# Optimization experiments

Hardware: AMD Instinct MI355X
Metric: run time of the kernel (lower is better)

Reference implementation:

```python
import jax, jax.numpy as jnp
import numpy as np
from jax import lax

V, H, M, OD, NL, S, B, KS = 32000, 1024, 16, 16, 4, 512, 16, 3
N = H // M          # 64
DN = OD * N         # 1024 (layernorm dim)
EPS = 1e-5


def _layernorm(x, g, b):
    mu = jnp.mean(x, axis=-1, keepdims=True)
    var = jnp.var(x, axis=-1, keepdims=True)
    return (x - mu) * lax.rsqrt(var + EPS) * g + b


def _conv(x, w, b):
    y = lax.conv_general_dilated(x, w, (1, 1), 'SAME',
                                 dimension_numbers=('NCHW', 'OIHW', 'NCHW'))
    return y + b[None, :, None, None]


def setup_inputs() -> dict:
    key = jax.random.key(0)
    ks = jax.random.split(key, 16)
    inp = {
        'x': jax.random.randint(ks[0], (B, S), 0, V),
        'emb_table': jax.random.normal(ks[1], (V, H), jnp.float32) * 0.02,
        'ln0_g': jnp.ones((H,), jnp.float32),
        'ln0_b': jnp.zeros((H,), jnp.float32),
        'qw': jax.random.normal(ks[2], (NL, OD, M, KS, KS), jnp.float32) * 0.05,
        'qb': jnp.zeros((NL, OD), jnp.float32),
        'kw': jax.random.normal(ks[3], (NL, OD, M, KS, KS), jnp.float32) * 0.05,
        'kb': jnp.zeros((NL, OD), jnp.float32),
        'vw': jax.random.normal(ks[4], (NL, OD, M, KS, KS), jnp.float32) * 0.05,
        'vb': jnp.zeros((NL, OD), jnp.float32),
        'lng': jnp.ones((NL, DN), jnp.float32),
        'lnb': jnp.zeros((NL, DN), jnp.float32),
        'cw': jax.random.normal(ks[5], (NL, M, OD, 3, 3), jnp.float32) * 0.05,
        'cb': jnp.zeros((NL, M), jnp.float32),
    }
    return inp


def reference(x, emb_table, ln0_g, ln0_b, qw, qb, kw, kb, vw, vb, lng, lnb, cw, cb):
    gelu = lambda t: jax.nn.gelu(t, approximate=False)  # torch nn.GELU default (erf)
    # embedding with padding_idx=0 (row forced to zero)
    table = emb_table.at[0].set(0.0)
    h = _layernorm(table[x], ln0_g, ln0_b)              # [B,S,H]
    h = h.reshape(B, S, M, N).transpose(0, 2, 1, 3)      # [B,M,S,N]
    outs = ()
    for i in range(NL):
        outs = outs + (h,)
        q = gelu(_conv(h, qw[i], qb[i]))                 # [B,OD,S,N]
        k = gelu(_conv(h, kw[i], kb[i]))
        v = gelu(_conv(h, vw[i], vb[i]))
        q2 = q.transpose(0, 2, 1, 3).reshape(B, S, DN)   # [B,S,OD*N]
        k2 = k.transpose(0, 1, 3, 2).reshape(B, DN, S)   # [B,OD*N,S]
        v2 = v.transpose(0, 2, 1, 3).reshape(B, S, DN)
        score = jax.nn.softmax(jnp.matmul(q2, k2), axis=0)  # softmax over batch (dim=0)
        o = jnp.matmul(score, v2)                        # [B,S,DN]
        o = _layernorm(o, lng[i], lnb[i])
        o = o.reshape(B, S, OD, N).transpose(0, 2, 1, 3)  # [B,OD,S,N]
        h = gelu(_conv(o, cw[i], cb[i])) + h             # residual, [B,M,S,N]
    return (h,) + outs
```

## Files before the change

### kernel.cpp

```cpp
#include <hip/hip_runtime.h>
#include <hip/hip_bf16.h>

typedef unsigned short u16;
typedef unsigned int   u32;
typedef short bf16x8 __attribute__((ext_vector_type(8)));
typedef float f32x4  __attribute__((ext_vector_type(4)));

#define SS 512
#define XSWZ(g) ((((g) & 7) << 6) | ((g) >> 3))

__device__ __forceinline__ float gelu_f(float v){
    float x  = v * 0.70710678118654752f;
    float ax = fabsf(x);
    float t  = __builtin_amdgcn_rcpf(fmaf(0.3275911f, ax, 1.0f));
    float poly = t*(0.254829592f + t*(-0.284496736f + t*(1.421413741f
               + t*(-1.453152027f + t*1.061405429f))));
    float e  = __expf(-x*x);
    float er = copysignf(1.0f - poly*e, x);
    return 0.5f*v*(1.0f + er);
}
__device__ __forceinline__ u16 bf16_rne(float v){
    u32 u = __float_as_uint(v);
    u32 r = u + 0x7FFF + ((u >> 16) & 1);
    return (u16)(r >> 16);
}
#define DYT(t) ((t)>=9 ? 0 : (t)/3)
#define DXT(t) ((t)>=9 ? 0 : (t)%3)

__global__ __launch_bounds__(256) void k_embed_ln(
    const int* __restrict__ x, const float* __restrict__ emb,
    const float* __restrict__ g, const float* __restrict__ bta,
    float* __restrict__ h, u16* __restrict__ hh, u16* __restrict__ hl)
{
    int bs = blockIdx.x;
    int b = bs >> 9, s = bs & 511;
    int t = x[bs];
    int tid = threadIdx.x;
    float v[4];
    #pragma unroll
    for (int j = 0; j < 4; ++j){
        int idx = tid + j*256;
        v[j] = (t == 0) ? 0.0f : emb[(size_t)t*1024 + idx];
    }
    float sum = v[0]+v[1]+v[2]+v[3];
    float sq  = v[0]*v[0]+v[1]*v[1]+v[2]*v[2]+v[3]*v[3];
    __shared__ float red[2][4];
    int lane = tid & 63, wid = tid >> 6;
    #pragma unroll
    for (int off = 32; off; off >>= 1){
        sum += __shfl_down(sum, off, 64);
        sq  += __shfl_down(sq,  off, 64);
    }
    if (lane == 0){ red[0][wid] = sum; red[1][wid] = sq; }
    __syncthreads();
    sum = red[0][0]+red[0][1]+red[0][2]+red[0][3];
    sq  = red[1][0]+red[1][1]+red[1][2]+red[1][3];
    float mean = sum * (1.0f/1024.0f);
    float var  = sq  * (1.0f/1024.0f) - mean*mean;
    float rs = rsqrtf(var + 1e-5f);
    #pragma unroll
    for (int j = 0; j < 4; ++j){
        int idx = tid + j*256;
        float y = (v[j]-mean)*rs*g[idx] + bta[idx];
        int m = idx >> 6, n = idx & 63;
        h[((size_t)(b*16 + m)*SS + s)*64 + n] = y;
        u16 hv = bf16_rne(y);
        u16 lv = bf16_rne(y - __uint_as_float((u32)hv<<16));
        size_t da = ((size_t)b*SS + s)*1024 + n*16 + m;
        hh[da] = hv; hl[da] = lv;
    }
}

__global__ __launch_bounds__(512,1) void k_conv_qkv(
    const u16* __restrict__ inh, const u16* __restrict__ inl,
    const float* __restrict__ qw, const float* __restrict__ qb,
    const float* __restrict__ kw, const float* __restrict__ kb,
    const float* __restrict__ vw, const float* __restrict__ vb,
    u16* __restrict__ qoh, u16* __restrict__ qol,
    u16* __restrict__ koh, u16* __restrict__ kol,
    u16* __restrict__ vT)
{
    int bid = XSWZ(blockIdx.x);
    int b  = bid >> 5;
    int y0 = (bid & 31) * 16;
    int tid = threadIdx.x;
    int w8 = tid >> 6, lane = tid & 63;
    int l15 = lane & 15, l4 = lane >> 4;
    int xt = w8 & 3, yh8 = (w8 >> 2) * 8;

    __shared__ u16 wq_h[2560], wq_l[2560], wk_h[2560], wk_l[2560], wv_h[2560];
    __shared__ u16 shi[18*68*24];
    __shared__ u16 slo[18*68*24];

    for (int idx = tid; idx < 2304; idx += 512){
        int o = idx / 144, rem = idx - o*144;
        int i = rem / 9, tap = rem - i*9;
        int dst = o*160 + tap*16 + i;
        float w0 = qw[idx];
        u16 h0 = bf16_rne(w0);
        wq_h[dst] = h0; wq_l[dst] = bf16_rne(w0 - __uint_as_float((u32)h0<<16));
        float w1 = kw[idx];
        u16 h1 = bf16_rne(w1);
        wk_h[dst] = h1; wk_l[dst] = bf16_rne(w1 - __uint_as_float((u32)h1<<16));
        wv_h[dst] = bf16_rne(vw[idx]);
    }
    if (tid < 256){
        int o = tid >> 4, kk = tid & 15;
        int dst = o*160 + 144 + kk;
        wq_h[dst]=0; wq_l[dst]=0; wk_h[dst]=0; wk_l[dst]=0; wv_h[dst]=0;
    }
    if (tid < 72){
        int y = tid >> 2, rr = tid & 3;
        int tc = (rr >> 1) ? 65 : 0;
        int h8 = (rr & 1) * 8;
        int ad = (y*68 + tc)*24 + h8;
        *(uint4*)&shi[ad] = make_uint4(0,0,0,0);
        *(uint4*)&slo[ad] = make_uint4(0,0,0,0);
    }
    for (int idx = tid; idx < 2304; idx += 512){
        int y = idx >> 7;
        int rem = idx & 127;
        int xx = rem >> 1, h8 = (rem & 1)*8;
        int gy = y0 - 1 + y;
        uint4 vh = make_uint4(0,0,0,0), vl = make_uint4(0,0,0,0);
        if (gy >= 0 && gy < SS){
            size_t ga = ((size_t)b*SS + gy)*1024 + xx*16 + h8;
            vh = *(const uint4*)(inh + ga);
            vl = *(const uint4*)(inl + ga);
        }
        int la = (y*68 + (xx+1))*24 + h8;
        *(uint4*)&shi[la] = vh;
        *(uint4*)&slo[la] = vl;
    }
    __syncthreads();

    bf16x8 aq_h[5], aq_l[5], ak_h[5], ak_l[5], av_h[5];
    #pragma unroll
    for (int p = 0; p < 5; ++p){
        int aad = l15*160 + p*32 + l4*8;
        aq_h[p] = *(const bf16x8*)&wq_h[aad];
        aq_l[p] = *(const bf16x8*)&wq_l[aad];
        ak_h[p] = *(const bf16x8*)&wk_h[aad];
        ak_l[p] = *(const bf16x8*)&wk_l[aad];
        av_h[p] = *(const bf16x8*)&wv_h[aad];
    }

    f32x4 accq[8], acck[8], accv[8];
    #pragma unroll
    for (int i = 0; i < 8; ++i){
        accq[i] = (f32x4){0.f,0.f,0.f,0.f};
        acck[i] = (f32x4){0.f,0.f,0.f,0.f};
        accv[i] = (f32x4){0.f,0.f,0.f,0.f};
    }
    int hsel = l4 >> 1;
    int i0 = (l4 & 1)*8;
    int xo = xt*16 + l15;

    #pragma unroll
    for (int p = 0; p < 5; ++p){
        int dy = hsel ? DYT(2*p+1) : DYT(2*p);
        int dx = hsel ? DXT(2*p+1) : DXT(2*p);
        int badd0 = ((dy + yh8)*68 + xo + dx)*24 + i0;
        #pragma unroll
        for (int yy = 0; yy < 8; ++yy){
            int bad = badd0 + yy*(68*24);
            bf16x8 bh = *(const bf16x8*)&shi[bad];
            bf16x8 bl = *(const bf16x8*)&slo[bad];
            accq[yy] = __builtin_amdgcn_mfma_f32_16x16x32_bf16(aq_h[p], bh, accq[yy],0,0,0);
            accq[yy] = __builtin_amdgcn_mfma_f32_16x16x32_bf16(aq_l[p], bh, accq[yy],0,0,0);
            accq[yy] = __builtin_amdgcn_mfma_f32_16x16x32_bf16(aq_h[p], bl, accq[yy],0,0,0);
            acck[yy] = __builtin_amdgcn_mfma_f32_16x16x32_bf16(ak_h[p], bh, acck[yy],0,0,0);
            acck[yy] = __builtin_amdgcn_mfma_f32_16x16x32_bf16(ak_l[p], bh, acck[yy],0,0,0);
            acck[yy] = __builtin_amdgcn_mfma_f32_16x16x32_bf16(ak_h[p], bl, acck[yy],0,0,0);
            accv[yy] = __builtin_amdgcn_mfma_f32_16x16x32_bf16(av_h[p], bh, accv[yy],0,0,0);
        }
    }

    float qbv[4], kbv[4], vbv[4];
    #pragma unroll
    for (int i = 0; i < 4; ++i){
        qbv[i] = qb[l4*4 + i];
        kbv[i] = kb[l4*4 + i];
        vbv[i] = vb[l4*4 + i];
    }
    union { u16 u[4][8]; uint4 q[4]; } vpk;
    #pragma unroll
    for (int yy = 0; yy < 8; ++yy){
        int y = y0 + yh8 + yy;
        u16 qh4[4], ql4[4], kh4[4], kl4[4];
        #pragma unroll
        for (int i = 0; i < 4; ++i){
            float vq = gelu_f(accq[yy][i] + qbv[i]);
            u16 hv = bf16_rne(vq);
            qh4[i] = hv; ql4[i] = bf16_rne(vq - __uint_as_float((u32)hv<<16));
            float vk = gelu_f(acck[yy][i] + kbv[i]);
            u16 kv = bf16_rne(vk);
            kh4[i] = kv; kl4[i] = bf16_rne(vk - __uint_as_float((u32)kv<<16));
            vpk.u[i][yy] = bf16_rne(gelu_f(accv[yy][i] + vbv[i]));
        }
        size_t oa = ((size_t)b*SS + y)*1024 + xo*16 + l4*4;
        *(uint2*)&qoh[oa] = make_uint2((u32)qh4[0]|((u32)qh4[1]<<16),(u32)qh4[2]|((u32)qh4[3]<<16));
        *(uint2*)&qol[oa] = make_uint2((u32)ql4[0]|((u32)ql4[1]<<16),(u32)ql4[2]|((u32)ql4[3]<<16));
        *(uint2*)&koh[oa] = make_uint2((u32)kh4[0]|((u32)kh4[1]<<16),(u32)kh4[2]|((u32)kh4[3]<<16));
        *(uint2*)&kol[oa] = make_uint2((u32)kl4[0]|((u32)kl4[1]<<16),(u32)kl4[2]|((u32)kl4[3]<<16));
    }
    #pragma unroll
    for (int i = 0; i < 4; ++i)
        *(uint4*)(vT + ((size_t)b*1024 + xo*16 + l4*4 + i)*SS + y0 + yh8) = vpk.q[i];
}

__global__ __launch_bounds__(512,1) void k_conv_ln_res2(
    const float* __restrict__ o_pre, const float* __restrict__ stats,
    const float* __restrict__ g, const float* __restrict__ bta,
    const float* __restrict__ w, const float* __restrict__ bias,
    const float* __restrict__ resid, float* __restrict__ outf,
    u16* __restrict__ outh, u16* __restrict__ outl)
{
    int bid = XSWZ(blockIdx.x);
    int b  = bid >> 5;
    int y0 = (bid & 31) * 16;
    int tid = threadIdx.x;
    int w8 = tid >> 6, lane = tid & 63;
    int l15 = lane & 15, l4 = lane >> 4;
    int xt = w8 & 3, yh8 = (w8 >> 2) * 8;

    __shared__ u16 whi[2560], wlo[2560];
    __shared__ u16 shi[18*68*24], slo[18*68*24];
    __shared__ float grem[1024], brem[1024];
    __shared__ float smu[18], srs[18];

    for (int idx = tid; idx < 2304; idx += 512){
        int o = idx / 144, rem = idx - o*144;
        int i = rem / 9, tap = rem - i*9;
        float wv = w[idx];
        u16 hv = bf16_rne(wv);
        int dst = o*160 + tap*16 + i;
        whi[dst] = hv;
        wlo[dst] = bf16_rne(wv - __uint_as_float((u32)hv<<16));
    }
    if (tid < 256){
        int o = tid >> 4, kk = tid & 15;
        whi[o*160 + 144 + kk] = 0;
        wlo[o*160 + 144 + kk] = 0;
    }
    for (int idx = tid; idx < 1024; idx += 512){
        int od = (idx & 15)*64 + (idx >> 4);
        grem[idx] = g[od];
        brem[idx] = bta[od];
    }
    if (tid < 18){
        int gy = y0 - 1 + tid;
        float mu = 0.f, rs = 0.f;
        if (gy >= 0 && gy < SS){
            float s = stats[2*((size_t)b*SS + gy)];
            float q = stats[2*((size_t)b*SS + gy) + 1];
            mu = s * (1.0f/1024.0f);
            float var = q * (1.0f/1024.0f) - mu*mu;
            rs = rsqrtf(var + 1e-5f);
        }
        smu[tid] = mu; srs[tid] = rs;
    }
    if (tid < 72){
        int y = tid >> 2, rr = tid & 3;
        int tc = (rr >> 1) ? 65 : 0;
        int h8 = (rr & 1) * 8;
        int ad = (y*68 + tc)*24 + h8;
        *(uint4*)&shi[ad] = make_uint4(0,0,0,0);
        *(uint4*)&slo[ad] = make_uint4(0,0,0,0);
    }
    __syncthreads();

    for (int idx = tid; idx < 4608; idx += 512){
        int y = idx >> 8;
        int rem = idx & 255;
        int xx = rem >> 2, cq = (rem & 3)*4;
        int gy = y0 - 1 + y;
        int la = (y*68 + xx + 1)*24 + cq;
        if (gy >= 0 && gy < SS){
            float4 vv = *(const float4*)(o_pre + ((size_t)b*SS + gy)*1024 + xx*16 + cq);
            float mu = smu[y], rs = srs[y];
            int dbase = xx*16 + cq;
            float va[4] = {vv.x, vv.y, vv.z, vv.w};
            u16 hh4[4], ll4[4];
            #pragma unroll
            for (int j = 0; j < 4; ++j){
                float yv = (va[j] - mu)*rs*grem[dbase + j] + brem[dbase + j];
                hh4[j] = bf16_rne(yv);
                ll4[j] = bf16_rne(yv - __uint_as_float((u32)hh4[j]<<16));
            }
            *(uint2*)&shi[la] = make_uint2((u32)hh4[0]|((u32)hh4[1]<<16),(u32)hh4[2]|((u32)hh4[3]<<16));
            *(uint2*)&slo[la] = make_uint2((u32)ll4[0]|((u32)ll4[1]<<16),(u32)ll4[2]|((u32)ll4[3]<<16));
        } else {
            *(uint2*)&shi[la] = make_uint2(0,0);
            *(uint2*)&slo[la] = make_uint2(0,0);
        }
    }
    __syncthreads();

    bf16x8 ah[5], al[5];
    #pragma unroll
    for (int p = 0; p < 5; ++p){
        int aad = l15*160 + p*32 + l4*8;
        ah[p] = *(const bf16x8*)&whi[aad];
        al[p] = *(const bf16x8*)&wlo[aad];
    }

    f32x4 acc[8];
    #pragma unroll
    for (int i = 0; i < 8; ++i) acc[i] = (f32x4){0.f,0.f,0.f,0.f};
    int hsel = l4 >> 1;
    int i0 = (l4 & 1)*8;
    int xo = xt*16 + l15;

    #pragma unroll
    for (int p = 0; p < 5; ++p){
        int dy = hsel ? DYT(2*p+1) : DYT(2*p);
        int dx = hsel ? DXT(2*p+1) : DXT(2*p);
        int badd0 = ((dy + yh8)*68 + xo + dx)*24 + i0;
        #pragma unroll
        for (int yy = 0; yy < 8; ++yy){
            int bad = badd0 + yy*(68*24);
            bf16x8 bh = *(const bf16x8*)&shi[bad];
            bf16x8 bl = *(const bf16x8*)&slo[bad];
            acc[yy] = __builtin_amdgcn_mfma_f32_16x16x32_bf16(ah[p], bh, acc[yy],0,0,0);
            acc[yy] = __builtin_amdgcn_mfma_f32_16x16x32_bf16(al[p], bh, acc[yy],0,0,0);
            acc[yy] = __builtin_amdgcn_mfma_f32_16x16x32_bf16(ah[p], bl, acc[yy],0,0,0);
        }
    }

    float bv[4];
    #pragma unroll
    for (int i = 0; i < 4; ++i) bv[i] = bias[l4*4 + i];
    #pragma unroll
    for (int yy = 0; yy < 8; ++yy){
        int y = y0 + yh8 + yy;
        float r[4];
        #pragma unroll
        for (int i = 0; i < 4; ++i) r[i] = gelu_f(acc[yy][i] + bv[i]);
        #pragma unroll
        for (int i = 0; i < 4; ++i){
            int o = l4*4 + i;
            size_t fa = ((size_t)(b*16 + o)*SS + y)*64 + xo;
            float hv = resid[fa] + r[i];
            outf[fa] = hv;
            r[i] = hv;
        }
        u16 hh_[4], ll_[4];
        #pragma unroll
        for (int i = 0; i < 4; ++i){
            hh_[i] = bf16_rne(r[i]);
            ll_[i] = bf16_rne(r[i] - __uint_as_float((u32)hh_[i]<<16));
        }
        size_t oa = ((size_t)b*SS + y)*1024 + xo*16 + l4*4;
        *(uint2*)&outh[oa] = make_uint2((u32)hh_[0]|((u32)hh_[1]<<16),(u32)hh_[2]|((u32)hh_[3]<<16));
        *(uint2*)&outl[oa] = make_uint2((u32)ll_[0]|((u32)ll_[1]<<16),(u32)ll_[2]|((u32)ll_[3]<<16));
    }
}

__global__ __launch_bounds__(256) void k_qk_mfma(
    const u16* __restrict__ qh, const u16* __restrict__ ql,
    const u16* __restrict__ kh, const u16* __restrict__ kl,
    float* __restrict__ score)
{
    int bid = XSWZ(blockIdx.x);
    int b = bid >> 5;
    int s1_0 = ((bid >> 3) & 3) * 128;
    int s2_0 = (bid & 7) * 64;
    __shared__ u16 Ah[128*64], Al[128*64], Bh[64*64], Bl[64*64];
    int tid = threadIdx.x;
    int w = tid >> 6, lane = tid & 63;
    int l15 = lane & 15, l4 = lane >> 4;
    f32x4 acc[2][4];
    #pragma unroll
    for (int r=0;r<2;++r)
        #pragma unroll
        for(int c=0;c<4;++c) acc[r][c] = (f32x4){0.f,0.f,0.f,0.f};

    for (int oc = 0; oc < 16; ++oc){
        size_t qbase = ((size_t)b*SS + s1_0)*1024 + oc*64;
        size_t kbase = ((size_t)b*SS + s2_0)*1024 + oc*64;
        #pragma unroll
        for (int i = 0; i < 4; ++i){
            int idx = tid + i*256;
            int r = idx >> 3, f = idx & 7;
            int dst = r*64 + ((f ^ (r & 7))*8);
            *(uint4*)&Ah[dst] = *(const uint4*)(qh + qbase + (size_t)r*1024 + f*8);
            *(uint4*)&Al[dst] = *(const uint4*)(ql + qbase + (size_t)r*1024 + f*8);
        }
        #pragma unroll
        for (int i = 0; i < 2; ++i){
            int idx = tid + i*256;
            int r = idx >> 3, f = idx & 7;
            int dst = r*64 + ((f ^ (r & 7))*8);
            *(uint4*)&Bh[dst] = *(const uint4*)(kh + kbase + (size_t)r*1024 + f*8);
            *(uint4*)&Bl[dst] = *(const uint4*)(kl + kbase + (size_t)r*1024 + f*8);
        }
        __syncthreads();
        #pragma unroll
        for (int ks = 0; ks < 2; ++ks){
            bf16x8 a_h[2], a_l[2];
            #pragma unroll
            for (int r=0;r<2;++r){
                int row = w*32 + r*16 + l15;
                int ad = row*64 + (((ks*4 + l4) ^ (row & 7))*8);
                a_h[r] = *(const bf16x8*)&Ah[ad];
                a_l[r] = *(const bf16x8*)&Al[ad];
            }
            #pragma unroll
            for (int c=0;c<4;++c){
                int row = c*16 + l15;
                int bd = row*64 + (((ks*4 + l4) ^ (row & 7))*8);
                bf16x8 b_h = *(const bf16x8*)&Bh[bd];
                bf16x8 b_l = *(const bf16x8*)&Bl[bd];
                #pragma unroll
                for (int r=0;r<2;++r){
                    acc[r][c] = __builtin_amdgcn_mfma_f32_16x16x32_bf16(a_h[r], b_h, acc[r][c],0,0,0);
                    acc[r][c] = __builtin_amdgcn_mfma_f32_16x16x32_bf16(a_l[r], b_h, acc[r][c],0,0,0);
                    acc[r][c] = __builtin_amdgcn_mfma_f32_16x16x32_bf16(a_h[r], b_l, acc[r][c],0,0,0);
                }
            }
        }
        __syncthreads();
    }
    #pragma unroll
    for (int r=0;r<2;++r)
        #pragma unroll
        for (int c=0;c<4;++c)
            #pragma unroll
            for (int i=0;i<4;++i){
                int s1 = s1_0 + w*32 + r*16 + l4*4 + i;
                int s2 = s2_0 + c*16 + l15;
                score[((size_t)b*SS + s1)*SS + s2] = acc[r][c][i];
            }
}

__global__ __launch_bounds__(256) void k_softmax_b(
    const float* __restrict__ score, u16* __restrict__ scb,
    float* __restrict__ stats)
{
    int sid = blockIdx.x*256 + threadIdx.x;
    if (sid < 16384) stats[sid] = 0.0f;
    float vals[16];
    float m = -1e30f;
    #pragma unroll
    for (int b = 0; b < 16; ++b){
        vals[b] = score[(size_t)b*SS*SS + sid];
        m = fmaxf(m, vals[b]);
    }
    float sum = 0.f;
    #pragma unroll
    for (int b = 0; b < 16; ++b){ vals[b] = __expf(vals[b]-m); sum += vals[b]; }
    float inv = 1.0f/sum;
    #pragma unroll
    for (int b = 0; b < 16; ++b) scb[(size_t)b*SS*SS + sid] = bf16_rne(vals[b]*inv);
}

__global__ __launch_bounds__(256) void k_sv_mfma(
    const u16* __restrict__ scb, const u16* __restrict__ vT,
    float* __restrict__ o, float* __restrict__ stats)
{
    int bid = XSWZ(blockIdx.x);
    int b = bid >> 5;
    int s1_0 = ((bid >> 3) & 3) * 128;
    int d0 = (bid & 7) * 128;
    __shared__ u16 As[128*64], Bs[128*64];
    int tid = threadIdx.x;
    int w = tid >> 6, lane = tid & 63;
    int l15 = lane & 15, l4 = lane >> 4;
    f32x4 acc[2][8];
    #pragma unroll
    for (int r=0;r<2;++r)
        #pragma unroll
        for(int c=0;c<8;++c) acc[r][c] = (f32x4){0.f,0.f,0.f,0.f};

    for (int st = 0; st < 8; ++st){
        int s2b = st*64;
        #pragma unroll
        for (int i = 0; i < 4; ++i){
            int idx = tid + i*256;
            int r = idx >> 3, f = idx & 7;
            int dst = r*64 + ((f ^ (r & 7))*8);
            *(uint4*)&As[dst] = *(const uint4*)(scb + ((size_t)b*SS + s1_0 + r)*SS + s2b + f*8);
            *(uint4*)&Bs[dst] = *(const uint4*)(vT + ((size_t)b*1024 + d0 + r)*SS + s2b + f*8);
        }
        __syncthreads();
        #pragma unroll
        for (int ks = 0; ks < 2; ++ks){
            bf16x8 a0[2];
            #pragma unroll
            for (int r=0;r<2;++r){
                int row = w*32 + r*16 + l15;
                a0[r] = *(const bf16x8*)&As[row*64 + (((ks*4 + l4) ^ (row & 7))*8)];
            }
            #pragma unroll
            for (int c=0;c<8;++c){
                int row = c*16 + l15;
                bf16x8 b0 = *(const bf16x8*)&Bs[row*64 + (((ks*4 + l4) ^ (row & 7))*8)];
                #pragma unroll
                for (int r=0;r<2;++r)
                    acc[r][c] = __builtin_amdgcn_mfma_f32_16x16x32_bf16(a0[r], b0, acc[r][c],0,0,0);
            }
        }
        __syncthreads();
    }
    #pragma unroll
    for (int r=0;r<2;++r)
        #pragma unroll
        for (int c=0;c<8;++c)
            #pragma unroll
            for (int i=0;i<4;++i){
                int s1 = s1_0 + w*32 + r*16 + l4*4 + i;
                o[((size_t)b*SS + s1)*1024 + d0 + c*16 + l15] = acc[r][c][i];
            }

    #pragma unroll
    for (int r=0;r<2;++r){
        #pragma unroll
        for (int i=0;i<4;++i){
            float s = 0.f, q = 0.f;
            #pragma unroll
            for (int c=0;c<8;++c){ float v = acc[r][c][i]; s += v; q += v*v; }
            #pragma unroll
            for (int m = 1; m <= 8; m <<= 1){
                s += __shfl_xor(s, m, 64);
                q += __shfl_xor(q, m, 64);
            }
            if (l15 == 0){
                int s1 = s1_0 + w*32 + r*16 + l4*4 + i;
                atomicAdd(&stats[2*((size_t)b*SS + s1)],     s);
                atomicAdd(&stats[2*((size_t)b*SS + s1) + 1], q);
            }
        }
    }
}

extern "C" void kernel_launch(void* const* d_in, const int* in_sizes, int n_in,
                              void* d_out, int out_size, void* d_ws, size_t ws_size,
                              hipStream_t stream)
{
    const int*   x    = (const int*)  d_in[0];
    const float* emb  = (const float*)d_in[1];
    const float* g0   = (const float*)d_in[2];
    const float* b0   = (const float*)d_in[3];
    const float* qw   = (const float*)d_in[4];
    const float* qb   = (const float*)d_in[5];
    const float* kw   = (const float*)d_in[6];
    const float* kb   = (const float*)d_in[7];
    const float* vw   = (const float*)d_in[8];
    const float* vb_  = (const float*)d_in[9];
    const float* lng  = (const float*)d_in[10];
    const float* lnb  = (const float*)d_in[11];
    const float* cw   = (const float*)d_in[12];
    const float* cb   = (const float*)d_in[13];
    float* out = (float*)d_out;

    const size_t TS = (size_t)16*16*512*64;
    u16* wsu = (u16*)d_ws;
    u16* hh = wsu + 0*TS;
    u16* hl = wsu + 1*TS;
    u16* qh = wsu + 2*TS;
    u16* ql = wsu + 3*TS;
    u16* kh = wsu + 4*TS;
    u16* kl = wsu + 5*TS;
    u16* vT = wsu + 6*TS;
    float* sc    = (float*)(wsu + 7*TS);
    u16*   scb   = qh;
    float* o_pre = (float*)(wsu + 4*TS);
    float* stats = (float*)(wsu + 3*TS);

    float* hbuf[5];
    hbuf[0] = out + 1*TS;
    hbuf[1] = out + 2*TS;
    hbuf[2] = out + 3*TS;
    hbuf[3] = out + 4*TS;
    hbuf[4] = out;

    k_embed_ln<<<8192, 256, 0, stream>>>(x, emb, g0, b0, hbuf[0], hh, hl);
    for (int i = 0; i < 4; ++i){
        k_conv_qkv<<<512, 512, 0, stream>>>(
            hh, hl, qw + i*2304, qb + i*16, kw + i*2304, kb + i*16,
            vw + i*2304, vb_ + i*16, qh, ql, kh, kl, vT);
        k_qk_mfma<<<512, 256, 0, stream>>>(qh, ql, kh, kl, sc);
        k_softmax_b<<<1024, 256, 0, stream>>>(sc, scb, stats);
        k_sv_mfma<<<512, 256, 0, stream>>>(scb, vT, o_pre, stats);
        k_conv_ln_res2<<<512, 512, 0, stream>>>(
            o_pre, stats, lng + i*1024, lnb + i*1024, cw + i*2304, cb + i*16,
            hbuf[i], hbuf[i+1], hh, hl);
    }
}
```

Measured before the change: 609.7 us.

## Precompute split-bf16 conv weights once; halve matmul tile height to double grid

Adds a small prep kernel that converts conv weights into hi/lo bf16 in the padded tap layout and permutes the layernorm gamma/beta, once per call for all layers. The two conv kernels then copy these into LDS with vector loads instead of converting per block. The QK and SV matmul kernels now use 64-row tiles instead of 128, launching 1024 blocks instead of 512 to improve occupancy and load balance across CUs, at the cost of reloading the B operand more often. The prep buffer sits at a fixed 160 MB workspace offset, which assumes the workspace is that large.

Result: slower. 671.2 us (+10.1%).

```diff
diff --git a/kernel.cpp b/kernel.cpp
--- a/kernel.cpp
+++ b/kernel.cpp
@@ -7,7 +7,9 @@
 typedef float f32x4  __attribute__((ext_vector_type(4)));
 
 #define SS 512
-#define XSWZ(g) ((((g) & 7) << 6) | ((g) >> 3))
+#define XSWZ(g)     ((((g) & 7) << 6) | ((g) >> 3))
+#define XSWZ1024(g) ((((g) & 7) << 7) | ((g) >> 3))
+#define WPREP_STRIDE 22016
 
 __device__ __forceinline__ float gelu_f(float v){
     float x  = v * 0.70710678118654752f;
@@ -27,6 +29,46 @@
 #define DYT(t) ((t)>=9 ? 0 : (t)/3)
 #define DXT(t) ((t)>=9 ? 0 : (t)%3)
 
+__global__ __launch_bounds__(256) void k_prep(
+    const float* __restrict__ qw, const float* __restrict__ kw,
+    const float* __restrict__ vw, const float* __restrict__ cw,
+    const float* __restrict__ lng, const float* __restrict__ lnb,
+    u16* __restrict__ wprep)
+{
+    int L = blockIdx.x;
+    int tid = threadIdx.x;
+    u16* base = wprep + L*WPREP_STRIDE;
+    const float* src[4] = {qw + L*2304, kw + L*2304, vw + L*2304, cw + L*2304};
+    const int offh[4] = {0, 5120, 10240, 12800};
+    const int offl[4] = {2560, 7680, -1, 15360};
+    for (int idx = tid; idx < 2304; idx += 256){
+        int o = idx / 144, rem = idx - o*144;
+        int i = rem / 9, tap = rem - i*9;
+        int dst = o*160 + tap*16 + i;
+        #pragma unroll
+        for (int a = 0; a < 4; ++a){
+            float wv = src[a][idx];
+            u16 hv = bf16_rne(wv);
+            base[offh[a] + dst] = hv;
+            if (offl[a] >= 0)
+                base[offl[a] + dst] = bf16_rne(wv - __uint_as_float((u32)hv<<16));
+        }
+    }
+    {
+        int o = tid >> 4, kk = tid & 15;
+        int d = o*160 + 144 + kk;
+        base[d]=0; base[2560+d]=0; base[5120+d]=0; base[7680+d]=0;
+        base[10240+d]=0; base[12800+d]=0; base[15360+d]=0;
+    }
+    float* gr = (float*)(base + 17920);
+    float* br = (float*)(base + 19968);
+    for (int idx = tid; idx < 1024; idx += 256){
+        int od = (idx & 15)*64 + (idx >> 4);
+        gr[idx] = lng[L*1024 + od];
+        br[idx] = lnb[L*1024 + od];
+    }
+}
+
 __global__ __launch_bounds__(256) void k_embed_ln(
     const int* __restrict__ x, const float* __restrict__ emb,
     const float* __restrict__ g, const float* __restrict__ bta,
@@ -73,9 +115,9 @@
 
 __global__ __launch_bounds__(512,1) void k_conv_qkv(
     const u16* __restrict__ inh, const u16* __restrict__ inl,
-    const float* __restrict__ qw, const float* __restrict__ qb,
-    const float* __restrict__ kw, const float* __restrict__ kb,
-    const float* __restrict__ vw, const float* __restrict__ vb,
+    const u16* __restrict__ wp,
+    const float* __restrict__ qb, const float* __restrict__ kb,
+    const float* __restrict__ vb,
     u16* __restrict__ qoh, u16* __restrict__ qol,
     u16* __restrict__ koh, u16* __restrict__ kol,
     u16* __restrict__ vT)
@@ -88,26 +130,16 @@
     int l15 = lane & 15, l4 = lane >> 4;
     int xt = w8 & 3, yh8 = (w8 >> 2) * 8;
 
-    __shared__ u16 wq_h[2560], wq_l[2560], wk_h[2560], wk_l[2560], wv_h[2560];
+    __shared__ __align__(16) u16 wq_h[2560], wq_l[2560], wk_h[2560], wk_l[2560], wv_h[2560];
     __shared__ u16 shi[18*68*24];
     __shared__ u16 slo[18*68*24];
 
-    for (int idx = tid; idx < 2304; idx += 512){
-        int o = idx / 144, rem = idx - o*144;
-        int i = rem / 9, tap = rem - i*9;
-        int dst = o*160 + tap*16 + i;
-        float w0 = qw[idx];
-        u16 h0 = bf16_rne(w0);
-        wq_h[dst] = h0; wq_l[dst] = bf16_rne(w0 - __uint_as_float((u32)h0<<16));
-        float w1 = kw[idx];
-        u16 h1 = bf16_rne(w1);
-        wk_h[dst] = h1; wk_l[dst] = bf16_rne(w1 - __uint_as_float((u32)h1<<16));
-        wv_h[dst] = bf16_rne(vw[idx]);
-    }
-    if (tid < 256){
-        int o = tid >> 4, kk = tid & 15;
-        int dst = o*160 + 144 + kk;
-        wq_h[dst]=0; wq_l[dst]=0; wk_h[dst]=0; wk_l[dst]=0; wv_h[dst]=0;
+    if (tid < 320){
+        ((uint4*)wq_h)[tid] = ((const uint4*)(wp        ))[tid];
+        ((uint4*)wq_l)[tid] = ((const uint4*)(wp +  2560))[tid];
+        ((uint4*)wk_h)[tid] = ((const uint4*)(wp +  5120))[tid];
+        ((uint4*)wk_l)[tid] = ((const uint4*)(wp +  7680))[tid];
+        ((uint4*)wv_h)[tid] = ((const uint4*)(wp + 10240))[tid];
     }
     if (tid < 72){
         int y = tid >> 2, rr = tid & 3;
@@ -211,8 +243,7 @@
 
 __global__ __launch_bounds__(512,1) void k_conv_ln_res2(
     const float* __restrict__ o_pre, const float* __restrict__ stats,
-    const float* __restrict__ g, const float* __restrict__ bta,
-    const float* __restrict__ w, const float* __restrict__ bias,
+    const u16* __restrict__ wp, const float* __restrict__ bias,
     const float* __restrict__ resid, float* __restrict__ outf,
     u16* __restrict__ outh, u16* __restrict__ outl)
 {
@@ -224,29 +255,18 @@
     int l15 = lane & 15, l4 = lane >> 4;
     int xt = w8 & 3, yh8 = (w8 >> 2) * 8;
 
-    __shared__ u16 whi[2560], wlo[2560];
+    __shared__ __align__(16) u16 whi[2560], wlo[2560];
     __shared__ u16 shi[18*68*24], slo[18*68*24];
-    __shared__ float grem[1024], brem[1024];
+    __shared__ __align__(16) float grem[1024], brem[1024];
     __shared__ float smu[18], srs[18];
 
-    for (int idx = tid; idx < 2304; idx += 512){
-        int o = idx / 144, rem = idx - o*144;
-        int i = rem / 9, tap = rem - i*9;
-        float wv = w[idx];
-        u16 hv = bf16_rne(wv);
-        int dst = o*160 + tap*16 + i;
-        whi[dst] = hv;
-        wlo[dst] = bf16_rne(wv - __uint_as_float((u32)hv<<16));
+    if (tid < 320){
+        ((uint4*)whi)[tid] = ((const uint4*)(wp + 12800))[tid];
+        ((uint4*)wlo)[tid] = ((const uint4*)(wp + 15360))[tid];
     }
     if (tid < 256){
-        int o = tid >> 4, kk = tid & 15;
-        whi[o*160 + 144 + kk] = 0;
-        wlo[o*160 + 144 + kk] = 0;
-    }
-    for (int idx = tid; idx < 1024; idx += 512){
-        int od = (idx & 15)*64 + (idx >> 4);
-        grem[idx] = g[od];
-        brem[idx] = bta[od];
+        ((float4*)grem)[tid] = ((const float4*)(wp + 17920))[tid];
+        ((float4*)brem)[tid] = ((const float4*)(wp + 19968))[tid];
     }
     if (tid < 18){
         int gy = y0 - 1 + tid;
@@ -260,8 +280,9 @@
         }
         smu[tid] = mu; srs[tid] = rs;
     }
-    if (tid < 72){
-        int y = tid >> 2, rr = tid & 3;
+    if (tid >= 64 && tid < 136){
+        int t2 = tid - 64;
+        int y = t2 >> 2, rr = t2 & 3;
         int tc = (rr >> 1) ? 65 : 0;
         int h8 = (rr & 1) * 8;
         int ad = (y*68 + tc)*24 + h8;
@@ -362,174 +383,150 @@
     const u16* __restrict__ kh, const u16* __restrict__ kl,
     float* __restrict__ score)
 {
-    int bid = XSWZ(blockIdx.x);
-    int b = bid >> 5;
-    int s1_0 = ((bid >> 3) & 3) * 128;
+    int bid = XSWZ1024(blockIdx.x);
+    int b = bid >> 6;
+    int s1_0 = ((bid >> 3) & 7) * 64;
     int s2_0 = (bid & 7) * 64;
-    __shared__ u16 Ah[128*64], Al[128*64], Bh[64*64], Bl[64*64];
+    __shared__ u16 Ah[64*64], Al[64*64], Bh[64*64], Bl[64*64];
     int tid = threadIdx.x;
     int w = tid >> 6, lane = tid & 63;
     int l15 = lane & 15, l4 = lane >> 4;
-    f32x4 acc[2][4];
-    #pragma unroll
-    for (int r=0;r<2;++r)
-        #pragma unroll
-        for(int c=0;c<4;++c) acc[r][c] = (f32x4){0.f,0.f,0.f,0.f};
+    f32x4 acc[4];
+    #pragma unroll
+    for (int c=0;c<4;++c) acc[c] = (f32x4){0.f,0.f,0.f,0.f};
 
     for (int oc = 0; oc < 16; ++oc){
         size_t qbase = ((size_t)b*SS + s1_0)*1024 + oc*64;
         size_t kbase = ((size_t)b*SS + s2_0)*1024 + oc*64;
         #pragma unroll
-        for (int i = 0; i < 4; ++i){
+        for (int i = 0; i < 2; ++i){
             int idx = tid + i*256;
             int r = idx >> 3, f = idx & 7;
             int dst = r*64 + ((f ^ (r & 7))*8);
             *(uint4*)&Ah[dst] = *(const uint4*)(qh + qbase + (size_t)r*1024 + f*8);
             *(uint4*)&Al[dst] = *(const uint4*)(ql + qbase + (size_t)r*1024 + f*8);
-        }
+            *(uint4*)&Bh[dst] = *(const uint4*)(kh + kbase + (size_t)r*1024 + f*8);
+            *(uint4*)&Bl[dst] = *(const uint4*)(kl + kbase + (size_t)r*1024 + f*8);
+        }
+        __syncthreads();
+        #pragma unroll
+        for (int ks = 0; ks < 2; ++ks){
+            int rowa = w*16 + l15;
+            int ad = rowa*64 + (((ks*4 + l4) ^ (rowa & 7))*8);
+            bf16x8 a_h = *(const bf16x8*)&Ah[ad];
+            bf16x8 a_l = *(const bf16x8*)&Al[ad];
+            #pragma unroll
+            for (int c=0;c<4;++c){
+                int rowb = c*16 + l15;
+                int bd = rowb*64 + (((ks*4 + l4) ^ (rowb & 7))*8);
+                bf16x8 b_h = *(const bf16x8*)&Bh[bd];
+                bf16x8 b_l = *(const bf16x8*)&Bl[bd];
+                acc[c] = __builtin_amdgcn_mfma_f32_16x16x32_bf16(a_h, b_h, acc[c],0,0,0);
+                acc[c] = __builtin_amdgcn_mfma_f32_16x16x32_bf16(a_l, b_h, acc[c],0,0,0);
+                acc[c] = __builtin_amdgcn_mfma_f32_16x16x32_bf16(a_h, b_l, acc[c],0,0,0);
+            }
+        }
+        __syncthreads();
+    }
+    #pragma unroll
+    for (int c=0;c<4;++c)
+        #pragma unroll
+        for (int i=0;i<4;++i){
+            int s1 = s1_0 + w*16 + l4*4 + i;
+            int s2 = s2_0 + c*16 + l15;
+            score[((size_t)b*SS + s1)*SS + s2] = acc[c][i];
+        }
+}
+
+__global__ __launch_bounds__(256) void k_softmax_b(
+    const float* __restrict__ score, u16* __restrict__ scb,
+    float* __restrict__ stats)
+{
+    int sid = blockIdx.x*256 + threadIdx.x;
+    if (sid < 16384) stats[sid] = 0.0f;
+    float vals[16];
+    float m = -1e30f;
+    #pragma unroll
+    for (int b = 0; b < 16; ++b){
+        vals[b] = score[(size_t)b*SS*SS + sid];
+        m = fmaxf(m, vals[b]);
+    }
+    float sum = 0.f;
+    #pragma unroll
+    for (int b = 0; b < 16; ++b){ vals[b] = __expf(vals[b]-m); sum += vals[b]; }
+    float inv = 1.0f/sum;
+    #pragma unroll
+    for (int b = 0; b < 16; ++b) scb[(size_t)b*SS*SS + sid] = bf16_rne(vals[b]*inv);
+}
+
+__global__ __launch_bounds__(256) void k_sv_mfma(
+    const u16* __restrict__ scb, const u16* __restrict__ vT,
+    float* __restrict__ o, float* __restrict__ stats)
+{
+    int bid = XSWZ1024(blockIdx.x);
+    int b = bid >> 6;
+    int s1_0 = ((bid >> 3) & 7) * 64;
+    int d0 = (bid & 7) * 128;
+    __shared__ u16 As[64*64], Bs[128*64];
+    int tid = threadIdx.x;
+    int w = tid >> 6, lane = tid & 63;
+    int l15 = lane & 15, l4 = lane >> 4;
+    f32x4 acc[8];
+    #pragma unroll
+    for(int c=0;c<8;++c) acc[c] = (f32x4){0.f,0.f,0.f,0.f};
+
+    for (int st = 0; st < 8; ++st){
+        int s2b = st*64;
         #pragma unroll
         for (int i = 0; i < 2; ++i){
             int idx = tid + i*256;
             int r = idx >> 3, f = idx & 7;
             int dst = r*64 + ((f ^ (r & 7))*8);
-            *(uint4*)&Bh[dst] = *(const uint4*)(kh + kbase + (size_t)r*1024 + f*8);
-            *(uint4*)&Bl[dst] = *(const uint4*)(kl + kbase + (size_t)r*1024 + f*8);
-        }
-        __syncthreads();
-        #pragma unroll
-        for (int ks = 0; ks < 2; ++ks){
-            bf16x8 a_h[2], a_l[2];
-            #pragma unroll
-            for (int r=0;r<2;++r){
-                int row = w*32 + r*16 + l15;
-                int ad = row*64 + (((ks*4 + l4) ^ (row & 7))*8);
-                a_h[r] = *(const bf16x8*)&Ah[ad];
-                a_l[r] = *(const bf16x8*)&Al[ad];
-            }
-            #pragma unroll
-            for (int c=0;c<4;++c){
-                int row = c*16 + l15;
-                int bd = row*64 + (((ks*4 + l4) ^ (row & 7))*8);
-                bf16x8 b_h = *(const bf16x8*)&Bh[bd];
-                bf16x8 b_l = *(const bf16x8*)&Bl[bd];
-                #pragma unroll
-                for (int r=0;r<2;++r){
-                    acc[r][c] = __builtin_amdgcn_mfma_f32_16x16x32_bf16(a_h[r], b_h, acc[r][c],0,0,0);
-                    acc[r][c] = __builtin_amdgcn_mfma_f32_16x16x32_bf16(a_l[r], b_h, acc[r][c],0,0,0);
-                    acc[r][c] = __builtin_amdgcn_mfma_f32_16x16x32_bf16(a_h[r], b_l, acc[r][c],0,0,0);
-                }
-            }
-        }
-        __syncthreads();
-    }
-    #pragma unroll
-    for (int r=0;r<2;++r)
-        #pragma unroll
-        for (int c=0;c<4;++c)
-            #pragma unroll
-            for (int i=0;i<4;++i){
-                int s1 = s1_0 + w*32 + r*16 + l4*4 + i;
-                int s2 = s2_0 + c*16 + l15;
-                score[((size_t)b*SS + s1)*SS + s2] = acc[r][c][i];
-            }
-}
-
-__global__ __launch_bounds__(256) void k_softmax_b(
-    const float* __restrict__ score, u16* __restrict__ scb,
-    float* __restrict__ stats)
-{
-    int sid = blockIdx.x*256 + threadIdx.x;
-    if (sid < 16384) stats[sid] = 0.0f;
-    float vals[16];
-    float m = -1e30f;
-    #pragma unroll
-    for (int b = 0; b < 16; ++b){
-        vals[b] = score[(size_t)b*SS*SS + sid];
-        m = fmaxf(m, vals[b]);
-    }
-    float sum = 0.f;
-    #pragma unroll
-    for (int b = 0; b < 16; ++b){ vals[b] = __expf(vals[b]-m); sum += vals[b]; }
-    float inv = 1.0f/sum;
-    #pragma unroll
-    for (int b = 0; b < 16; ++b) scb[(size_t)b*SS*SS + sid] = bf16_rne(vals[b]*inv);
-}
-
-__global__ __launch_bounds__(256) void k_sv_mfma(
-    const u16* __restrict__ scb, const u16* __restrict__ vT,
-    float* __restrict__ o, float* __restrict__ stats)
-{
-    int bid = XSWZ(blockIdx.x);
-    int b = bid >> 5;
-    int s1_0 = ((bid >> 3) & 3) * 128;
-    int d0 = (bid & 7) * 128;
-    __shared__ u16 As[128*64], Bs[128*64];
-    int tid = threadIdx.x;
-    int w = tid >> 6, lane = tid & 63;
-    int l15 = lane & 15, l4 = lane >> 4;
-    f32x4 acc[2][8];
-    #pragma unroll
-    for (int r=0;r<2;++r)
-        #pragma unroll
-        for(int c=0;c<8;++c) acc[r][c] = (f32x4){0.f,0.f,0.f,0.f};
-
-    for (int st = 0; st < 8; ++st){
-        int s2b = st*64;
+            *(uint4*)&As[dst] = *(const uint4*)(scb + ((size_t)b*SS + s1_0 + r)*SS + s2b + f*8);
+        }
         #pragma unroll
         for (int i = 0; i < 4; ++i){
             int idx = tid + i*256;
             int r = idx >> 3, f = idx & 7;
             int dst = r*64 + ((f ^ (r & 7))*8);
-            *(uint4*)&As[dst] = *(const uint4*)(scb + ((size_t)b*SS + s1_0 + r)*SS + s2b + f*8);
             *(uint4*)&Bs[dst] = *(const uint4*)(vT + ((size_t)b*1024 + d0 + r)*SS + s2b + f*8);
         }
         __syncthreads();
         #pragma unroll
         for (int ks = 0; ks < 2; ++ks){
-            bf16x8 a0[2];
-            #pragma unroll
-            for (int r=0;r<2;++r){
-                int row = w*32 + r*16 + l15;
-                a0[r] = *(const bf16x8*)&As[row*64 + (((ks*4 + l4) ^ (row & 7))*8)];
-            }
+            int rowa = w*16 + l15;
+            bf16x8 a0 = *(const bf16x8*)&As[rowa*64 + (((ks*4 + l4) ^ (rowa & 7))*8)];
             #pragma unroll
             for (int c=0;c<8;++c){
-                int row = c*16 + l15;
-                bf16x8 b0 = *(const bf16x8*)&Bs[row*64 + (((ks*4 + l4) ^ (row & 7))*8)];
-                #pragma unroll
-                for (int r=0;r<2;++r)
-                    acc[r][c] = __builtin_amdgcn_mfma_f32_16x16x32_bf16(a0[r], b0, acc[r][c],0,0,0);
+                int rowb = c*16 + l15;
+                bf16x8 b0 = *(const bf16x8*)&Bs[rowb*64 + (((ks*4 + l4) ^ (rowb & 7))*8)];
+                acc[c] = __builtin_amdgcn_mfma_f32_16x16x32_bf16(a0, b0, acc[c],0,0,0);
             }
         }
         __syncthreads();
     }
     #pragma unroll
-    for (int r=0;r<2;++r)
-        #pragma unroll
-        for (int c=0;c<8;++c)
-            #pragma unroll
-            for (int i=0;i<4;++i){
-                int s1 = s1_0 + w*32 + r*16 + l4*4 + i;
-                o[((size_t)b*SS + s1)*1024 + d0 + c*16 + l15] = acc[r][c][i];
-            }
-
-    #pragma unroll
-    for (int r=0;r<2;++r){
+    for (int c=0;c<8;++c)
         #pragma unroll
         for (int i=0;i<4;++i){
-            float s = 0.f, q = 0.f;
-            #pragma unroll
-            for (int c=0;c<8;++c){ float v = acc[r][c][i]; s += v; q += v*v; }
-            #pragma unroll
-            for (int m = 1; m <= 8; m <<= 1){
-                s += __shfl_xor(s, m, 64);
-                q += __shfl_xor(q, m, 64);
-            }
-            if (l15 == 0){
-                int s1 = s1_0 + w*32 + r*16 + l4*4 + i;
-                atomicAdd(&stats[2*((size_t)b*SS + s1)],     s);
-                atomicAdd(&stats[2*((size_t)b*SS + s1) + 1], q);
-            }
+            int s1 = s1_0 + w*16 + l4*4 + i;
+            o[((size_t)b*SS + s1)*1024 + d0 + c*16 + l15] = acc[c][i];
+        }
+
+    #pragma unroll
+    for (int i=0;i<4;++i){
+        float s = 0.f, q = 0.f;
+        #pragma unroll
+        for (int c=0;c<8;++c){ float v = acc[c][i]; s += v; q += v*v; }
+        #pragma unroll
+        for (int m = 1; m <= 8; m <<= 1){
+            s += __shfl_xor(s, m, 64);
+            q += __shfl_xor(q, m, 64);
+        }
+        if (l15 == 0){
+            int s1 = s1_0 + w*16 + l4*4 + i;
+            atomicAdd(&stats[2*((size_t)b*SS + s1)],     s);
+            atomicAdd(&stats[2*((size_t)b*SS + s1) + 1], q);
         }
     }
 }
@@ -567,6 +564,7 @@
     u16*   scb   = qh;
     float* o_pre = (float*)(wsu + 4*TS);
     float* stats = (float*)(wsu + 3*TS);
+    u16* wprep = (u16*)((char*)d_ws + ((size_t)160 << 20));
 
     float* hbuf[5];
     hbuf[0] = out + 1*TS;
@@ -575,16 +573,16 @@
     hbuf[3] = out + 4*TS;
     hbuf[4] = out;
 
+    k_prep<<<4, 256, 0, stream>>>(qw, kw, vw, cw, lng, lnb, wprep);
     k_embed_ln<<<8192, 256, 0, stream>>>(x, emb, g0, b0, hbuf[0], hh, hl);
     for (int i = 0; i < 4; ++i){
+        const u16* wp = wprep + i*WPREP_STRIDE;
         k_conv_qkv<<<512, 512, 0, stream>>>(
-            hh, hl, qw + i*2304, qb + i*16, kw + i*2304, kb + i*16,
-            vw + i*2304, vb_ + i*16, qh, ql, kh, kl, vT);
-        k_qk_mfma<<<512, 256, 0, stream>>>(qh, ql, kh, kl, sc);
+            hh, hl, wp, qb + i*16, kb + i*16, vb_ + i*16, qh, ql, kh, kl, vT);
+        k_qk_mfma<<<1024, 256, 0, stream>>>(qh, ql, kh, kl, sc);
         k_softmax_b<<<1024, 256, 0, stream>>>(sc, scb, stats);
-        k_sv_mfma<<<512, 256, 0, stream>>>(scb, vT, o_pre, stats);
+        k_sv_mfma<<<1024, 256, 0, stream>>>(scb, vT, o_pre, stats);
         k_conv_ln_res2<<<512, 512, 0, stream>>>(
-            o_pre, stats, lng + i*1024, lnb + i*1024, cw + i*2304, cb + i*16,
-            hbuf[i], hbuf[i+1], hh, hl);
-    }
-}
+            o_pre, stats, wp, cb + i*16, hbuf[i], hbuf[i+1], hh, hl);
+    }
+}
```
